# Kernel optimization log

Measured on AMD Instinct MI355X. Metric: run time of the kernel, lower is better.

The kernel has to match this reference:

```python
import jax, jax.numpy as jnp
import numpy as np

NUM_LAYERS = 4
CODEBOOK_SIZE = 2048
DIM = 256
N = 32768
BETA = 0.25
EPS = 1e-12  # F.normalize eps


def setup_inputs() -> dict:
    key = jax.random.key(0)
    kx, kc = jax.random.split(key)
    x = jax.random.normal(kx, (N, DIM), dtype=jnp.float32)
    # nn.Embedding default init: N(0, 1)
    codebooks = jax.random.normal(kc, (NUM_LAYERS, CODEBOOK_SIZE, DIM), dtype=jnp.float32)
    return {"x": x, "codebooks": codebooks}


def reference(x, codebooks):
    sg = jax.lax.stop_gradient
    residual = x
    all_indices = []
    decoded = jnp.zeros_like(x)
    total_loss = jnp.zeros((), dtype=x.dtype)
    n_elem = x.size
    for layer in range(NUM_LAYERS):
        cb = codebooks[layer]                      # [K, D] (raw, used for gather)
        norm = jnp.linalg.norm(cb, axis=-1, keepdims=True)
        cbn = cb / jnp.maximum(norm, EPS)          # L2-normalized, used for distances
        # squared L2 distances; argmin is invariant to the sqrt in torch.cdist
        d2 = (
            jnp.sum(residual * residual, axis=-1, keepdims=True)
            - 2.0 * residual @ cbn.T
            + jnp.sum(cbn * cbn, axis=-1)
        )                                          # [N, K]
        idx = jnp.argmin(d2, axis=-1)              # [N]
        all_indices.append(idx)
        q = cb[idx]                                # [N, D] gather from RAW codebook
        codebook_loss = jnp.sum((residual - sg(q)) ** 2) / n_elem
        commitment_loss = jnp.sum((sg(residual) - q) ** 2) / n_elem
        total_loss = total_loss + codebook_loss + BETA * commitment_loss
        decoded = decoded + q
        # residual = residual - (residual + sg(q - residual)) == sg(residual - q)
        residual = sg(residual - q)
    stru_ids = jnp.stack(all_indices, axis=1)      # [N, L]
    return stru_ids, decoded, total_loss
```

## Files before the change

kernel.cpp:

```cpp
#include <hip/hip_runtime.h>
#include <math.h>

#define L_NUM 4
#define K_CB  2048
#define D_DIM 256
#define N_ROWS 32768
#define CAP 56
#define WACC  0.12f
#define WACC2 0.125f

typedef _Float16 half8 __attribute__((ext_vector_type(8)));
typedef _Float16 half4v __attribute__((ext_vector_type(4)));
typedef float f32x16 __attribute__((ext_vector_type(16)));

__device__ __forceinline__ void gl_lds16(const void* g, void* l) {
  __builtin_amdgcn_global_load_lds(
      (const __attribute__((address_space(1))) void*)g,
      (__attribute__((address_space(3))) void*)l, 16, 0, 0);
}
__device__ __forceinline__ unsigned fenc(float f) {
  unsigned u = __float_as_uint(f);
  return (u & 0x80000000u) ? ~u : (u | 0x80000000u);
}
__device__ __forceinline__ float fdec(unsigned k) {
  unsigned u = (k & 0x80000000u) ? (k ^ 0x80000000u) : ~k;
  return __uint_as_float(u);
}

__device__ __forceinline__ float tmax64(const f32x16& a, const f32x16& b,
                                        const f32x16& c, const f32x16& d) {
  float m[16];
  #pragma unroll
  for (int i = 0; i < 16; ++i)
    m[i] = fmaxf(fmaxf(a[i], b[i]), fmaxf(c[i], d[i]));
  #pragma unroll
  for (int s2 = 8; s2 >= 1; s2 >>= 1)
    #pragma unroll
    for (int i = 0; i < s2; ++i) m[i] = fmaxf(m[i], m[i + s2]);
  return m[0];
}

__global__ __launch_bounds__(64)
void prep_all_kernel(const float* __restrict__ cb,
                     float* __restrict__ cbn,
                     double* __restrict__ c2d,
                     _Float16* __restrict__ cb16) {
  const int b = blockIdx.x;
  const int k = b & 2047, l = b >> 11;
  const int lane = threadIdx.x;
  float4 v = reinterpret_cast<const float4*>(cb + (size_t)b * D_DIM)[lane];
  float s = v.x*v.x + v.y*v.y + v.z*v.z + v.w*v.w;
  #pragma unroll
  for (int m = 1; m < 64; m <<= 1) s += __shfl_xor(s, m, 64);
  const float den = fmaxf(sqrtf(s), 1e-12f);
  v.x /= den; v.y /= den; v.z /= den; v.w /= den;
  reinterpret_cast<float4*>(cbn + (size_t)b * D_DIM)[lane] = v;
  double td = (double)v.x*v.x + (double)v.y*v.y + (double)v.z*v.z + (double)v.w*v.w;
  #pragma unroll
  for (int m = 1; m < 64; m <<= 1) td += __shfl_xor(td, m, 64);
  if (lane == 0) c2d[b] = td;
  half4v h;
  h[0] = (_Float16)v.x; h[1] = (_Float16)v.y; h[2] = (_Float16)v.z; h[3] = (_Float16)v.w;
  const int tile = k >> 9, col = k & 511;
  const int kchunk = lane >> 3;
  const int sslot  = (lane >> 1) & 3;
  const int rem    = (lane & 1) * 4;
  const size_t off = (size_t)l * (K_CB * D_DIM)
                   + (size_t)(tile * 8 + kchunk) * 16384
                   + (size_t)sslot * 4096 + (size_t)col * 8 + rem;
  *(half4v*)(cb16 + off) = h;
}

__global__ __launch_bounds__(512, 2)
void rq_fused_kernel(const float* __restrict__ x,
                     const float* __restrict__ cb,
                     const float* __restrict__ cbn,
                     const double* __restrict__ c2d,
                     const _Float16* __restrict__ cb16,
                     float* __restrict__ out_ids,
                     float* __restrict__ out_dec,
                     double* __restrict__ dloss) {
  extern __shared__ char sm[];
  _Float16* A16   = (_Float16*)sm;
  _Float16* Bs    = (_Float16*)(sm + 65536);
  unsigned* cp    = (unsigned*)(sm + 131072);
  int*      cn    = (int*)(sm + 131072 + 128*CAP*4);
  unsigned* gmax  = (unsigned*)((char*)cn + 512);
  unsigned* bestp = (unsigned*)((char*)gmax + 512);

  const int t = threadIdx.x;
  const int wid = t >> 6, ln = t & 63;
  const int l31 = ln & 31, hl = ln >> 5;
  const int rowg = wid >> 2, colg = wid & 3;
  const int urow = t >> 2, qo = (t & 3) * 64;
  const int row0 = blockIdx.x * 128;
  const int mrow0 = rowg * 64 + l31, mrow1 = mrow0 + 32;

  float r[64];
  {
    const float4* xg = (const float4*)(x + (size_t)(row0 + urow) * D_DIM + qo);
    #pragma unroll
    for (int i = 0; i < 16; ++i) {
      const float4 a = xg[i];
      r[i*4+0]=a.x; r[i*4+1]=a.y; r[i*4+2]=a.z; r[i*4+3]=a.w;
    }
  }
  #pragma unroll
  for (int j = 0; j < 8; ++j) {
    half8 h;
    #pragma unroll
    for (int e = 0; e < 8; ++e) h[e] = (_Float16)r[j*8+e];
    const int slot = (t & 3) * 8 + j;
    *(half8*)(A16 + slot*1024 + urow*8) = h;
  }
  if (t < 128) { cn[t] = 0; gmax[t] = 0u; bestp[t] = 0u; }
  int id0 = 0, id1 = 0, id2 = 0, id3 = 0;
  double lloss = 0.0;

  {
    const char* B0 = (const char*)cb16;
    #pragma unroll
    for (int i = 0; i < 4; ++i)
      gl_lds16(B0 + t*16 + i*8192, (char*)Bs + t*16 + i*8192);
  }

  #pragma unroll 1
  for (int l = 0; l < L_NUM; ++l) {
    const char* Bimg = (const char*)cb16 + (size_t)l * (K_CB * D_DIM * 2);
    __syncthreads();

    f32x16 acc[4][2];

    #pragma unroll 1
    for (int g = 0; g < 32; ++g) {
      if ((g & 7) == 0) {
        #pragma unroll
        for (int bi = 0; bi < 4; ++bi)
          #pragma unroll
          for (int ai = 0; ai < 2; ++ai)
            #pragma unroll
            for (int e = 0; e < 16; ++e) acc[bi][ai][e] = 0.f;
      }
      if (g < 31) {
        char* dst = (char*)Bs + ((g + 1) & 1) * 32768;
        const char* src = Bimg + (size_t)(g + 1) * 32768;
        #pragma unroll
        for (int i = 0; i < 4; ++i)
          gl_lds16(src + t*16 + i*8192, dst + t*16 + i*8192);
      }
      const _Float16* Bb = Bs + (g & 1) * 16384;
      const int cK = g & 7;
      #pragma unroll
      for (int ks2 = 0; ks2 < 2; ++ks2) {
        const int sa = cK*4 + ks2*2 + hl;
        const int sb = ks2*2 + hl;
        half8 af[2], bf[4];
        af[0] = *(const half8*)(A16 + sa*1024 + mrow0*8);
        af[1] = *(const half8*)(A16 + sa*1024 + mrow1*8);
        #pragma unroll
        for (int bi = 0; bi < 4; ++bi) {
          const int col = colg*128 + bi*32 + l31;
          bf[bi] = *(const half8*)(Bb + sb*4096 + col*8);
        }
        #pragma unroll
        for (int bi = 0; bi < 4; ++bi) {
          acc[bi][0] = __builtin_amdgcn_mfma_f32_32x32x16_f16(bf[bi], af[0], acc[bi][0], 0, 0, 0);
          acc[bi][1] = __builtin_amdgcn_mfma_f32_32x32x16_f16(bf[bi], af[1], acc[bi][1], 0, 0, 0);
        }
      }
      if ((g & 7) == 7) {
        const int ct = g >> 3;
        #pragma unroll
        for (int ai = 0; ai < 2; ++ai) {
          const int mrow = ai ? mrow1 : mrow0;
          const float m = ai ? tmax64(acc[0][1], acc[1][1], acc[2][1], acc[3][1])
                             : tmax64(acc[0][0], acc[1][0], acc[2][0], acc[3][0]);
          atomicMax(&gmax[mrow], fenc(m));
          const float thr = fdec(gmax[mrow]) - WACC;
          #pragma unroll
          for (int bi = 0; bi < 4; ++bi)
            #pragma unroll
            for (int rg = 0; rg < 16; ++rg) {
              const float v = acc[bi][ai][rg];
              if (v >= thr) {
                const unsigned q = (unsigned)((v + 64.f) * 16384.f);
                const unsigned cidx = (unsigned)(ct*512 + colg*128 + bi*32
                                                 + 4*hl + (rg & 3) + 8*(rg >> 2));
                const unsigned pk = (q << 11) | cidx;
                atomicMax(&bestp[mrow], pk);
                const int slot = atomicAdd(&cn[mrow], 1);
                if (slot < CAP) cp[mrow*CAP + slot] = pk;
              }
            }
        }
      }
      __syncthreads();
    }

    if (l < 3) {
      const char* Bn = (const char*)cb16 + (size_t)(l + 1) * (K_CB * D_DIM * 2);
      #pragma unroll
      for (int i = 0; i < 4; ++i)
        gl_lds16(Bn + t*16 + i*8192, (char*)Bs + t*16 + i*8192);
    }

    {
      const float thr2 = fdec(gmax[urow]) - WACC2;
      const int m = min(cn[urow], CAP);
      double bsc = (double)INFINITY; int bidx = 0x7fffffff;
      #pragma unroll 1
      for (int j = 0; j <= m; ++j) {
        const unsigned p = (j < m) ? cp[urow*CAP + j] : bestp[urow];
        const float v = (float)(p >> 11) * (1.f/16384.f) - 64.f;
        if (j < m && v < thr2) continue;
        const int cidx = (int)(p & 2047u);
        const float4* cpn = (const float4*)(cbn + ((size_t)l*K_CB + cidx)*D_DIM + qo);
        double s = 0.0;
        #pragma unroll
        for (int i = 0; i < 16; ++i) {
          const float4 a = cpn[i];
          s = fma((double)r[i*4+0], (double)a.x, s);
          s = fma((double)r[i*4+1], (double)a.y, s);
          s = fma((double)r[i*4+2], (double)a.z, s);
          s = fma((double)r[i*4+3], (double)a.w, s);
        }
        s += __shfl_xor(s, 1, 64);
        s += __shfl_xor(s, 2, 64);
        const double sc = -2.0 * s + c2d[l*K_CB + cidx];
        if (sc < bsc || (sc == bsc && cidx < bidx)) { bsc = sc; bidx = cidx; }
      }
      bidx &= 2047;
      if (l == 0) id0 = bidx; else if (l == 1) id1 = bidx;
      else if (l == 2) id2 = bidx; else id3 = bidx;
      if ((t & 3) == 0) out_ids[(size_t)(row0 + urow)*L_NUM + l] = (float)bidx;

      const float4* qg = (const float4*)(cb + ((size_t)l*K_CB + bidx)*D_DIM + qo);
      #pragma unroll
      for (int i = 0; i < 16; ++i) {
        const float4 q = qg[i];
        r[i*4+0] -= q.x; r[i*4+1] -= q.y; r[i*4+2] -= q.z; r[i*4+3] -= q.w;
        lloss += (double)r[i*4+0]*r[i*4+0] + (double)r[i*4+1]*r[i*4+1]
               + (double)r[i*4+2]*r[i*4+2] + (double)r[i*4+3]*r[i*4+3];
      }
      if (l < 3) {
        #pragma unroll
        for (int j = 0; j < 8; ++j) {
          half8 h;
          #pragma unroll
          for (int e = 0; e < 8; ++e) h[e] = (_Float16)r[j*8+e];
          const int slot = (t & 3) * 8 + j;
          *(half8*)(A16 + slot*1024 + urow*8) = h;
        }
      }
    }
    __syncthreads();
    if (l < 3 && t < 128) { cn[t] = 0; gmax[t] = 0u; bestp[t] = 0u; }
  }

  {
    float dec[64];
    #pragma unroll
    for (int l2 = 0; l2 < L_NUM; ++l2) {
      const int idl = (l2 == 0) ? id0 : (l2 == 1) ? id1 : (l2 == 2) ? id2 : id3;
      const float4* qg = (const float4*)(cb + ((size_t)l2*K_CB + idl)*D_DIM + qo);
      #pragma unroll
      for (int i = 0; i < 16; ++i) {
        const float4 q = qg[i];
        if (l2 == 0) { dec[i*4+0]=q.x; dec[i*4+1]=q.y; dec[i*4+2]=q.z; dec[i*4+3]=q.w; }
        else { dec[i*4+0]+=q.x; dec[i*4+1]+=q.y; dec[i*4+2]+=q.z; dec[i*4+3]+=q.w; }
      }
    }
    float4* dg = (float4*)(out_dec + (size_t)(row0 + urow)*D_DIM + qo);
    #pragma unroll
    for (int i = 0; i < 16; ++i)
      dg[i] = make_float4(dec[i*4+0], dec[i*4+1], dec[i*4+2], dec[i*4+3]);
  }

  double* lw = (double*)cp;
  #pragma unroll
  for (int m = 1; m < 64; m <<= 1) lloss += __shfl_xor(lloss, m, 64);
  if (ln == 0) lw[wid] = lloss;
  __syncthreads();
  if (t == 0) {
    double s2 = 0.0;
    #pragma unroll
    for (int j = 0; j < 8; ++j) s2 += lw[j];
    atomicAdd(dloss, s2);
  }
}

__global__ void rq_fin_kernel(const double* __restrict__ dls, float* __restrict__ out_loss) {
  out_loss[0] = (float)(dls[0] * 1.25 / 8388608.0);
}

extern "C" void kernel_launch(void* const* d_in, const int* in_sizes, int n_in,
                              void* d_out, int out_size, void* d_ws, size_t ws_size,
                              hipStream_t stream) {
  const float* x  = (const float*)d_in[0];
  const float* cb = (const float*)d_in[1];
  float* out      = (float*)d_out;
  float* out_ids  = out;
  float* out_dec  = out + (size_t)N_ROWS * L_NUM;
  float* out_loss = out_dec + (size_t)N_ROWS * D_DIM;

  char* w = (char*)d_ws;
  double* dls = (double*)w;                   w += 256;
  double* c2d = (double*)w;                   w += (size_t)L_NUM*K_CB*8;
  float* cbn = (float*)w;                     w += (size_t)L_NUM*K_CB*D_DIM*4;
  _Float16* cb16 = (_Float16*)w;              w += (size_t)L_NUM*K_CB*D_DIM*2;

  hipMemsetAsync(dls, 0, sizeof(double), stream);
  prep_all_kernel<<<L_NUM*K_CB, 64, 0, stream>>>(cb, cbn, c2d, cb16);

  const size_t smem = 65536 + 65536 + 128*CAP*4 + 512 + 512 + 512;
  hipFuncSetAttribute(reinterpret_cast<const void*>(rq_fused_kernel),
                      hipFuncAttributeMaxDynamicSharedMemorySize, (int)smem);
  rq_fused_kernel<<<N_ROWS/128, 512, smem, stream>>>(x, cb, cbn, c2d, cb16,
                                                     out_ids, out_dec, dls);
  rq_fin_kernel<<<1, 1, 0, stream>>>(dls, out_loss);
}
```

Baseline: 351.2 us.

## Read codebook fragments directly from global memory instead of LDS double buffer

Removes the LDS double-buffered staging of the fp16 codebook tiles and has each wave load its B fragments straight from global memory (relying on L2/cache reuse across waves and blocks). This drops the per-iteration __syncthreads and shrinks shared memory by 64 KB, which may let more blocks fit per CU. The trade-off is more global/L2 traffic and exposed load latency in front of the MFMA loop, with no explicit prefetch.

```diff
diff --git a/kernel.cpp b/kernel.cpp
--- a/kernel.cpp
+++ b/kernel.cpp
@@ -13,11 +13,6 @@
 typedef _Float16 half4v __attribute__((ext_vector_type(4)));
 typedef float f32x16 __attribute__((ext_vector_type(16)));
 
-__device__ __forceinline__ void gl_lds16(const void* g, void* l) {
-  __builtin_amdgcn_global_load_lds(
-      (const __attribute__((address_space(1))) void*)g,
-      (__attribute__((address_space(3))) void*)l, 16, 0, 0);
-}
 __device__ __forceinline__ unsigned fenc(float f) {
   unsigned u = __float_as_uint(f);
   return (u & 0x80000000u) ? ~u : (u | 0x80000000u);
@@ -82,9 +77,8 @@
                      double* __restrict__ dloss) {
   extern __shared__ char sm[];
   _Float16* A16   = (_Float16*)sm;
-  _Float16* Bs    = (_Float16*)(sm + 65536);
-  unsigned* cp    = (unsigned*)(sm + 131072);
-  int*      cn    = (int*)(sm + 131072 + 128*CAP*4);
+  unsigned* cp    = (unsigned*)(sm + 65536);
+  int*      cn    = (int*)((char*)cp + 128*CAP*4);
   unsigned* gmax  = (unsigned*)((char*)cn + 512);
   unsigned* bestp = (unsigned*)((char*)gmax + 512);
 
@@ -117,16 +111,9 @@
   int id0 = 0, id1 = 0, id2 = 0, id3 = 0;
   double lloss = 0.0;
 
-  {
-    const char* B0 = (const char*)cb16;
-    #pragma unroll
-    for (int i = 0; i < 4; ++i)
-      gl_lds16(B0 + t*16 + i*8192, (char*)Bs + t*16 + i*8192);
-  }
-
   #pragma unroll 1
   for (int l = 0; l < L_NUM; ++l) {
-    const char* Bimg = (const char*)cb16 + (size_t)l * (K_CB * D_DIM * 2);
+    const _Float16* Bimg = cb16 + (size_t)l * (K_CB * D_DIM);
     __syncthreads();
 
     f32x16 acc[4][2];
@@ -141,14 +128,7 @@
             #pragma unroll
             for (int e = 0; e < 16; ++e) acc[bi][ai][e] = 0.f;
       }
-      if (g < 31) {
-        char* dst = (char*)Bs + ((g + 1) & 1) * 32768;
-        const char* src = Bimg + (size_t)(g + 1) * 32768;
-        #pragma unroll
-        for (int i = 0; i < 4; ++i)
-          gl_lds16(src + t*16 + i*8192, dst + t*16 + i*8192);
-      }
-      const _Float16* Bb = Bs + (g & 1) * 16384;
+      const _Float16* Bc = Bimg + (size_t)g * 16384;
       const int cK = g & 7;
       #pragma unroll
       for (int ks2 = 0; ks2 < 2; ++ks2) {
@@ -160,7 +140,7 @@
         #pragma unroll
         for (int bi = 0; bi < 4; ++bi) {
           const int col = colg*128 + bi*32 + l31;
-          bf[bi] = *(const half8*)(Bb + sb*4096 + col*8);
+          bf[bi] = *(const half8*)(Bc + sb*4096 + col*8);
         }
         #pragma unroll
         for (int bi = 0; bi < 4; ++bi) {
@@ -194,15 +174,8 @@
             }
         }
       }
-      __syncthreads();
-    }
-
-    if (l < 3) {
-      const char* Bn = (const char*)cb16 + (size_t)(l + 1) * (K_CB * D_DIM * 2);
-      #pragma unroll
-      for (int i = 0; i < 4; ++i)
-        gl_lds16(Bn + t*16 + i*8192, (char*)Bs + t*16 + i*8192);
-    }
+    }
+    __syncthreads();
 
     {
       const float thr2 = fdec(gmax[urow]) - WACC2;
@@ -312,7 +285,7 @@
   hipMemsetAsync(dls, 0, sizeof(double), stream);
   prep_all_kernel<<<L_NUM*K_CB, 64, 0, stream>>>(cb, cbn, c2d, cb16);
 
-  const size_t smem = 65536 + 65536 + 128*CAP*4 + 512 + 512 + 512;
+  const size_t smem = 65536 + 128*CAP*4 + 512 + 512 + 512;
   hipFuncSetAttribute(reinterpret_cast<const void*>(rq_fused_kernel),
                       hipFuncAttributeMaxDynamicSharedMemorySize, (int)smem);
   rq_fused_kernel<<<N_ROWS/128, 512, smem, stream>>>(x, cb, cbn, c2d, cb16,
```

New measurement: 554.3 us. 57.8% more time.
